# Kernel tuning notes

Hardware: AMD Instinct MI355X
Metric: run time of the kernel (lower is better)

## Reference

```python
import jax, jax.numpy as jnp
import numpy as np

DIM = 2048
K_DIM = 2048
HQ = 16          # query heads
HKV = 4          # kv heads
HD = DIM // HQ   # head dim = 128
KV_DIM = HD * HKV
MAX_LEN = 4096
THETA = 10000.0
ROPE_FACTOR = 8.0
CAUSAL = True
SCALE = HD ** -0.5


def rope_cos_sin(n):
    # mirrors generate_sin_cos_pos_emb (rope_factor > 1 branch)
    idx = jnp.arange(0, HD, 2, dtype=jnp.float32) / HD
    seq_len_eff = max(n, MAX_LEN)  # static python ints
    base_adjustment = (ROPE_FACTOR * seq_len_eff / MAX_LEN - (ROPE_FACTOR - 1.0)) ** (HD / (HD - 2))
    inv_freq = 1.0 / (THETA * base_adjustment) ** idx
    pos = jnp.arange(n, dtype=jnp.float32)
    if not CAUSAL:
        pos = pos - (n - 1) // 2
    freqs = pos[:, None] * inv_freq[None, :]          # [n, HD/2]
    emb = jnp.concatenate([freqs, freqs], axis=-1)    # [n, HD]
    return jnp.cos(emb), jnp.sin(emb)


def rotate_half(x):
    x1, x2 = jnp.split(x, 2, axis=-1)
    return jnp.concatenate([-x2, x1], axis=-1)


def setup_inputs() -> dict:
    key = jax.random.key(0)
    ks = jax.random.split(key, 11)
    B, N = 2, 2048
    s = 0.02
    return {
        "query": jax.random.normal(ks[0], (B, N, DIM), jnp.float32),
        "key": jax.random.normal(ks[1], (B, N, K_DIM), jnp.float32),
        "value": jax.random.normal(ks[2], (B, N, K_DIM), jnp.float32),
        "Wq": jax.random.normal(ks[3], (DIM, DIM), jnp.float32) * s,
        "bq": jnp.zeros((DIM,), jnp.float32),
        "Wk": jax.random.normal(ks[4], (KV_DIM, K_DIM), jnp.float32) * s,
        "bk": jnp.zeros((KV_DIM,), jnp.float32),
        "Wv": jax.random.normal(ks[5], (KV_DIM, K_DIM), jnp.float32) * s,
        "bv": jnp.zeros((KV_DIM,), jnp.float32),
        "Wo": jax.random.normal(ks[6], (DIM, DIM), jnp.float32) * s,
        "bo": jnp.zeros((DIM,), jnp.float32),
    }


def reference(query, key, value, Wq, bq, Wk, bk, Wv, bv, Wo, bo):
    b, n, _ = query.shape
    q = query @ Wq.T + bq                       # [b, n, DIM]
    k = key @ Wk.T + bk                         # [b, n, KV_DIM]
    v = value @ Wv.T + bv                       # [b, n, KV_DIM]
    q = q.reshape(b, n, HQ, HD).transpose(0, 2, 1, 3)    # [b, HQ, n, d]
    k = k.reshape(b, n, HKV, HD).transpose(0, 2, 1, 3)   # [b, HKV, n, d]
    v = v.reshape(b, n, HKV, HD).transpose(0, 2, 1, 3)
    cos, sin = rope_cos_sin(n)                  # [n, HD] each, broadcast over b,h
    q = q * cos + rotate_half(q) * sin
    k = k * cos + rotate_half(k) * sin
    g = HQ // HKV
    qg = q.reshape(b, HKV, g, n, HD)            # group query heads per kv head
    scores = jnp.einsum('bhgnd,bhsd->bhgns', qg * SCALE, k)  # [b, HKV, g, n, s]
    if CAUSAL:
        causal = jnp.tril(jnp.ones((n, n), dtype=bool))
        scores = jnp.where(causal[None, None, None], scores, jnp.finfo(scores.dtype).min)
    attn = jax.nn.softmax(scores, axis=-1)
    out = jnp.einsum('bhgns,bhsd->bhgnd', attn, v)           # [b, HKV, g, n, d]
    out = out.reshape(b, HQ, n, HD).transpose(0, 2, 1, 3).reshape(b, n, DIM)
    return out @ Wo.T + bo
```

## Files before the change

### kernel.cpp

```cpp
#include <hip/hip_runtime.h>
#include <cstdint>


typedef __bf16 bf16_t;
typedef __attribute__((ext_vector_type(8))) __bf16 bf16x8;
typedef __attribute__((ext_vector_type(4))) float f32x4;

#define B_    2
#define N_    2048
#define DIM_  2048
#define HQ_   16
#define HKV_  4
#define HD_   128
#define KVD_  512
#define SCALE_ 0.08838834764831845f

static __device__ __forceinline__ void ld_g2l(void* lds, const void* g) {
  __builtin_amdgcn_global_load_lds((__attribute__((address_space(1))) void*)g,
                                   (__attribute__((address_space(3))) void*)lds,
                                   16, 0, 0);
}

static __device__ __forceinline__ f32x4 vmax4(f32x4 a, f32x4 b) {
  f32x4 r;
  r[0] = fmaxf(a[0], b[0]); r[1] = fmaxf(a[1], b[1]);
  r[2] = fmaxf(a[2], b[2]); r[3] = fmaxf(a[3], b[3]);
  return r;
}

__global__ void k_sincos(float* __restrict__ cosT, float* __restrict__ sinT) {
  int idx = blockIdx.x * 256 + threadIdx.x;
  int i = idx & 63;
  int n = idx >> 6;
  float inv = expf(-(float)i * (9.210340371976184f / 64.0f));
  float ang = (float)n * inv;
  cosT[idx] = cosf(ang);
  sinT[idx] = sinf(ang);
}

__global__ void k_cvt4(const float* __restrict__ s0, bf16_t* __restrict__ d0, int n0,
                       const float* __restrict__ s1, bf16_t* __restrict__ d1, int n1,
                       const float* __restrict__ s2, bf16_t* __restrict__ d2, int n2,
                       const float* __restrict__ s3, bf16_t* __restrict__ d3, int n3)
{
  int i = (blockIdx.x * 256 + threadIdx.x) * 4;
  const float* s; bf16_t* d; int off;
  if (i < n0)                     { s = s0; d = d0; off = i; }
  else if (i < n0 + n1)           { s = s1; d = d1; off = i - n0; }
  else if (i < n0 + n1 + n2)      { s = s2; d = d2; off = i - n0 - n1; }
  else if (i < n0 + n1 + n2 + n3) { s = s3; d = d3; off = i - n0 - n1 - n2; }
  else return;
  f32x4 v = *(const f32x4*)(s + off);
  union { bf16_t h[4]; uint2 u; } pk;
  pk.h[0] = (bf16_t)v[0]; pk.h[1] = (bf16_t)v[1];
  pk.h[2] = (bf16_t)v[2]; pk.h[3] = (bf16_t)v[3];
  *(uint2*)(d + off) = pk.u;
}

__global__ __launch_bounds__(256, 2) void k_gemm_qkv(
    const float* __restrict__ q, const bf16_t* __restrict__ Wqb,
    const float* __restrict__ bq, bf16_t* __restrict__ Qp,
    const float* __restrict__ k, const bf16_t* __restrict__ Wkb,
    const float* __restrict__ bk, bf16_t* __restrict__ Kp,
    const float* __restrict__ v, const bf16_t* __restrict__ Wvb,
    const float* __restrict__ bv, bf16_t* __restrict__ Vp)
{
  __shared__ bf16_t As[128 * 64];
  __shared__ bf16_t Bs[2][128 * 64];
  const int z = blockIdx.z;
  if (z != 0 && blockIdx.y >= 2) return;
  const float* A; const bf16_t* W; const float* bias; bf16_t* C; int Nn;
  if (z == 0)      { A = q; W = Wqb; bias = bq; C = Qp; Nn = 2048; }
  else if (z == 1) { A = k; W = Wkb; bias = bk; C = Kp; Nn = 512; }
  else             { A = v; W = Wvb; bias = bv; C = Vp; Nn = 512; }

  const int tid  = threadIdx.x;
  const int lane = tid & 63;
  const int wave = tid >> 6;
  const int l15  = lane & 15;
  const int lg   = lane >> 4;
  const int bm = blockIdx.x;
  const int bn0 = blockIdx.y * 2, bn1 = bn0 + 1;
  const int wr = (wave >> 1) * 64, wc = (wave & 1) * 64;
  const int K = 2048;

  f32x4 acc0[4][4] = {};
  f32x4 acc1[4][4] = {};

  uint8_t* AsB = (uint8_t*)As;
  uint8_t* Bs0 = (uint8_t*)Bs[0];
  uint8_t* Bs1 = (uint8_t*)Bs[1];
  const uint8_t* Wb0 = (const uint8_t*)W + (size_t)(bn0 * 128) * K * 2;
  const uint8_t* Wb1 = (const uint8_t*)W + (size_t)(bn1 * 128) * K * 2;

  f32x4 arLo[4], arHi[4];

  auto loadA = [&](int k0) {
#pragma unroll
    for (int i = 0; i < 4; ++i) {
      int c = i * 256 + tid;
      int row = c >> 3;
      int k8  = (c & 7) * 8;
      const float* ap = A + (size_t)(bm * 128 + row) * K + k0 + k8;
      arLo[i] = *(const f32x4*)ap;
      arHi[i] = *(const f32x4*)(ap + 4);
    }
  };
  auto writeA = [&]() {
#pragma unroll
    for (int i = 0; i < 4; ++i) {
      int c = i * 256 + tid;
      int row = c >> 3;
      int k8  = (c & 7) * 8;
      bf16x8 va;
      f32x4 lo = arLo[i], hi = arHi[i];
      va[0] = (bf16_t)lo[0]; va[1] = (bf16_t)lo[1];
      va[2] = (bf16_t)lo[2]; va[3] = (bf16_t)lo[3];
      va[4] = (bf16_t)hi[0]; va[5] = (bf16_t)hi[1];
      va[6] = (bf16_t)hi[2]; va[7] = (bf16_t)hi[3];
      int sw = (k8 * 2) ^ ((row & 7) << 4);
      *(bf16x8*)(AsB + row * 128 + sw) = va;
    }
  };

  loadA(0);

  for (int k0 = 0; k0 < K; k0 += 64) {
#pragma unroll
    for (int r = 0; r < 4; ++r) {
      int o = r * 4096 + wave * 1024 + lane * 16;
      int row = o >> 7;
      int colB = (o & 127) ^ ((row & 7) << 4);
      size_t goff = (size_t)row * (K * 2) + (size_t)k0 * 2 + colB;
      ld_g2l(Bs0 + r * 4096 + wave * 1024, Wb0 + goff);
      ld_g2l(Bs1 + r * 4096 + wave * 1024, Wb1 + goff);
    }
    writeA();
    __syncthreads();
    if (k0 + 64 < K) loadA(k0 + 64);
    __builtin_amdgcn_s_setprio(1);
#pragma unroll
    for (int kk = 0; kk < 2; ++kk) {
      const int koff = kk * 64 + (lg << 4);
      bf16x8 fa[4], fb[4];
#pragma unroll
      for (int fi = 0; fi < 4; ++fi) {
        int row = wr + fi * 16 + l15;
        fa[fi] = *(const bf16x8*)(AsB + row * 128 + (koff ^ ((row & 7) << 4)));
      }
#pragma unroll
      for (int fj = 0; fj < 4; ++fj) {
        int row = wc + fj * 16 + l15;
        fb[fj] = *(const bf16x8*)(Bs0 + row * 128 + (koff ^ ((row & 7) << 4)));
      }
#pragma unroll
      for (int fi = 0; fi < 4; ++fi)
#pragma unroll
        for (int fj = 0; fj < 4; ++fj)
          acc0[fi][fj] = __builtin_amdgcn_mfma_f32_16x16x32_bf16(
              fa[fi], fb[fj], acc0[fi][fj], 0, 0, 0);
#pragma unroll
      for (int fj = 0; fj < 4; ++fj) {
        int row = wc + fj * 16 + l15;
        fb[fj] = *(const bf16x8*)(Bs1 + row * 128 + (koff ^ ((row & 7) << 4)));
      }
#pragma unroll
      for (int fi = 0; fi < 4; ++fi)
#pragma unroll
        for (int fj = 0; fj < 4; ++fj)
          acc1[fi][fj] = __builtin_amdgcn_mfma_f32_16x16x32_bf16(
              fa[fi], fb[fj], acc1[fi][fj], 0, 0, 0);
    }
    __builtin_amdgcn_s_setprio(0);
    __syncthreads();
  }

  const int r0 = lg * 4;
#pragma unroll
  for (int fi = 0; fi < 4; ++fi) {
#pragma unroll
    for (int rr = 0; rr < 4; ++rr) {
      int grow = bm * 128 + wr + fi * 16 + r0 + rr;
      size_t rowoff = (size_t)grow * Nn;
#pragma unroll
      for (int fj = 0; fj < 4; ++fj) {
        int gc0 = bn0 * 128 + wc + fj * 16 + l15;
        int gc1 = bn1 * 128 + wc + fj * 16 + l15;
        C[rowoff + gc0] = (bf16_t)(acc0[fi][fj][rr] + bias[gc0]);
        C[rowoff + gc1] = (bf16_t)(acc1[fi][fj][rr] + bias[gc1]);
      }
    }
  }
}

__global__ __launch_bounds__(256, 4) void k_gemm_o(
    const bf16_t* __restrict__ Ain, const bf16_t* __restrict__ Wob,
    const float* __restrict__ bo, float* __restrict__ out)
{
  __shared__ bf16_t As[128 * 64];
  __shared__ bf16_t Bs[128 * 64];
  const int tid  = threadIdx.x;
  const int lane = tid & 63;
  const int wave = tid >> 6;
  const int l15  = lane & 15;
  const int lg   = lane >> 4;
  const int bm = blockIdx.x, bn = blockIdx.y;
  const int wr = (wave >> 1) * 64, wc = (wave & 1) * 64;
  const int K = 2048, N = 2048;

  f32x4 acc[4][4] = {};
  uint8_t* AsB = (uint8_t*)As;
  uint8_t* BsB = (uint8_t*)Bs;
  const uint8_t* Wbase = (const uint8_t*)Wob + (size_t)(bn * 128) * K * 2;
  const uint8_t* Abase = (const uint8_t*)Ain + (size_t)(bm * 128) * K * 2;

  for (int k0 = 0; k0 < K; k0 += 64) {
    for (int r = 0; r < 4; ++r) {
      int o = r * 4096 + wave * 1024 + lane * 16;
      int row = o >> 7;
      int colB = (o & 127) ^ ((row & 7) << 4);
      size_t goff = (size_t)row * (K * 2) + (size_t)k0 * 2 + colB;
      ld_g2l(BsB + r * 4096 + wave * 1024, Wbase + goff);
      ld_g2l(AsB + r * 4096 + wave * 1024, Abase + goff);
    }
    __syncthreads();
    for (int kk = 0; kk < 2; ++kk) {
      const int koff = kk * 64 + (lg << 4);
      bf16x8 fa[4], fb[4];
      for (int fi = 0; fi < 4; ++fi) {
        int row = wr + fi * 16 + l15;
        fa[fi] = *(const bf16x8*)(AsB + row * 128 + (koff ^ ((row & 7) << 4)));
      }
      for (int fj = 0; fj < 4; ++fj) {
        int row = wc + fj * 16 + l15;
        fb[fj] = *(const bf16x8*)(BsB + row * 128 + (koff ^ ((row & 7) << 4)));
      }
      for (int fi = 0; fi < 4; ++fi)
        for (int fj = 0; fj < 4; ++fj)
          acc[fi][fj] = __builtin_amdgcn_mfma_f32_16x16x32_bf16(
              fa[fi], fb[fj], acc[fi][fj], 0, 0, 0);
    }
    __syncthreads();
  }

  const int r0 = lg * 4;
  for (int fi = 0; fi < 4; ++fi) {
    for (int rr = 0; rr < 4; ++rr) {
      int grow = bm * 128 + wr + fi * 16 + r0 + rr;
      size_t rowoff = (size_t)grow * N;
      for (int fj = 0; fj < 4; ++fj) {
        int gcol = bn * 128 + wc + fj * 16 + l15;
        out[rowoff + gcol] = acc[fi][fj][rr] + bo[gcol];
      }
    }
  }
}

__global__ void k_ropek_transv(bf16_t* __restrict__ Kp,
                               const float* __restrict__ cosT,
                               const float* __restrict__ sinT,
                               const bf16_t* __restrict__ Vp,
                               bf16_t* __restrict__ Vt)
{
  __shared__ bf16_t tile[64][72];
  const int tid = threadIdx.x;
  if (blockIdx.x < 512) {
    int idx = blockIdx.x * 256 + tid;
    int j = idx & 7;
    int h = (idx >> 3) & 3;
    int row = idx >> 5;
    int n = row & (N_ - 1);
    int d0 = j * 8;
    const float* cp = cosT + (n << 6) + d0;
    const float* sp = sinT + (n << 6) + d0;
    f32x4 c0 = *(const f32x4*)cp,  c1 = *(const f32x4*)(cp + 4);
    f32x4 s0 = *(const f32x4*)sp,  s1 = *(const f32x4*)(sp + 4);
    bf16_t* xb = Kp + (size_t)row * 512 + (h << 7) + d0;
    bf16x8 x1 = *(const bf16x8*)xb;
    bf16x8 x2 = *(const bf16x8*)(xb + 64);
    bf16x8 o1, o2;
#pragma unroll
    for (int e = 0; e < 8; ++e) {
      float c = e < 4 ? c0[e] : c1[e - 4];
      float s = e < 4 ? s0[e] : s1[e - 4];
      float a = (float)x1[e], bvl = (float)x2[e];
      o1[e] = (bf16_t)(a * c - bvl * s);
      o2[e] = (bf16_t)(bvl * c + a * s);
    }
    *(bf16x8*)xb = o1;
    *(bf16x8*)(xb + 64) = o2;
    return;
  }
  const int bid = blockIdx.x - 512;
  const int r0 = (bid & 63) * 64;
  const int d0 = (bid >> 6) * 64;
  for (int r = 0; r < 2; ++r) {
    int n = r * 32 + (tid >> 3);
    int dc = (tid & 7) * 8;
    *(uint4*)&tile[n][dc] = *(const uint4*)(Vp + (size_t)(r0 + n) * KVD_ + d0 + dc);
  }
  __syncthreads();
  const int b = r0 >> 11;
  const int nseq = r0 & (N_ - 1);
  for (int r = 0; r < 2; ++r) {
    int dd = r * 32 + (tid >> 3);
    int nc = (tid & 7) * 8;
    int dglob = d0 + dd;
    int hkv = dglob >> 7, dloc = dglob & 127;
    union { bf16_t h[8]; uint4 v; } pk;
    for (int j = 0; j < 8; ++j) pk.h[j] = tile[nc + j][dd];
    size_t drow = (size_t)(b * HKV_ + hkv) * 128 + dloc;
    *(uint4*)(Vt + drow * N_ + nseq + nc) = pk.v;
  }
}

__global__ __launch_bounds__(256, 2) void k_attn(
    const bf16_t* __restrict__ Qp, const bf16_t* __restrict__ Kp,
    const bf16_t* __restrict__ Vt, bf16_t* __restrict__ AO,
    const float* __restrict__ cosT, const float* __restrict__ sinT)
{
  __shared__ bf16_t Ks[2][64 * 128];
  __shared__ bf16_t Vs[2][128 * 64];
  __shared__ bf16_t Ps[4][16 * 72];
  const int tid = threadIdx.x, lane = tid & 63, wave = tid >> 6;
  const int l15 = lane & 15, lg = lane >> 4;
  const int bx = (blockIdx.y < 16) ? (15 - (int)blockIdx.x) : (int)blockIdx.x;
  const int qtile = bx * 4 + wave;
  const int bh = blockIdx.y;
  const int b = bh >> 4, hq = bh & 15, hkv = hq >> 2;

  bf16x8 qf[2][4];
#pragma unroll
  for (int rf = 0; rf < 2; ++rf) {
    int n = qtile * 32 + rf * 16 + l15;
    size_t qrow = (size_t)b * N_ + n;
    const uint8_t* qb = (const uint8_t*)Qp + (qrow * DIM_ + (size_t)hq * HD_) * 2 + lg * 16;
#pragma unroll
    for (int ks = 0; ks < 4; ++ks)
      qf[rf][ks] = *(const bf16x8*)(qb + ks * 64);
    const float* cb = cosT + n * 64 + lg * 8;
    const float* sb = sinT + n * 64 + lg * 8;
    f32x4 c0a = *(const f32x4*)cb,        c0b = *(const f32x4*)(cb + 4);
    f32x4 c1a = *(const f32x4*)(cb + 32), c1b = *(const f32x4*)(cb + 36);
    f32x4 s0a = *(const f32x4*)sb,        s0b = *(const f32x4*)(sb + 4);
    f32x4 s1a = *(const f32x4*)(sb + 32), s1b = *(const f32x4*)(sb + 36);
#pragma unroll
    for (int e = 0; e < 8; ++e) {
      float c0 = e < 4 ? c0a[e] : c0b[e - 4], s0 = e < 4 ? s0a[e] : s0b[e - 4];
      float c1 = e < 4 ? c1a[e] : c1b[e - 4], s1 = e < 4 ? s1a[e] : s1b[e - 4];
      float a0 = (float)qf[rf][0][e], b0 = (float)qf[rf][2][e];
      float a1 = (float)qf[rf][1][e], b1 = (float)qf[rf][3][e];
      qf[rf][0][e] = (bf16_t)((a0 * c0 - b0 * s0) * SCALE_);
      qf[rf][2][e] = (bf16_t)((b0 * c0 + a0 * s0) * SCALE_);
      qf[rf][1][e] = (bf16_t)((a1 * c1 - b1 * s1) * SCALE_);
      qf[rf][3][e] = (bf16_t)((b1 * c1 + a1 * s1) * SCALE_);
    }
  }

  float m[2] = {-1e30f, -1e30f};
  float ln[2] = {0.f, 0.f};
  f32x4 o[2][8] = {};

  const uint8_t* KpB = (const uint8_t*)Kp + ((size_t)b * N_ * KVD_ + (size_t)hkv * HD_) * 2;
  const uint8_t* VtB = (const uint8_t*)Vt + (size_t)(b * HKV_ + hkv) * HD_ * (size_t)N_ * 2;
  uint8_t* PwB = (uint8_t*)Ps[wave];

  const int Tw   = qtile / 2 + 1;
  const int Tmax = 2 * bx + 2;

  auto stage = [&](int buf, int t) {
    uint8_t* KsB = (uint8_t*)Ks[buf];
    uint8_t* VsB = (uint8_t*)Vs[buf];
#pragma unroll
    for (int r = 0; r < 4; ++r) {
      int o16 = r * 4096 + wave * 1024 + lane * 16;
      int row = o16 >> 8;
      int colB = (o16 & 255) ^ ((row & 7) << 4);
      ld_g2l(KsB + r * 4096 + wave * 1024,
             KpB + (size_t)(t * 64 + row) * (KVD_ * 2) + colB);
    }
#pragma unroll
    for (int r = 0; r < 4; ++r) {
      int o16 = r * 4096 + wave * 1024 + lane * 16;
      int dd = o16 >> 7;
      int colB = (o16 & 127) ^ ((dd & 7) << 4);
      ld_g2l(VsB + r * 4096 + wave * 1024,
             VtB + (size_t)dd * (N_ * 2) + t * 128 + colB);
    }
  };

  stage(0, 0);
  __syncthreads();
  int cur = 0;

  for (int t = 0; t < Tmax; ++t) {
    if (t + 1 < Tmax) stage(cur ^ 1, t + 1);

    if (t < Tw) {
      const uint8_t* KsB = (const uint8_t*)Ks[cur];
      const uint8_t* VsB = (const uint8_t*)Vs[cur];

      f32x4 s4[2][4] = {};
      __builtin_amdgcn_s_setprio(1);
#pragma unroll
      for (int ks = 0; ks < 4; ++ks) {
        int koff = ks * 64 + lg * 16;
#pragma unroll
        for (int kb = 0; kb < 4; ++kb) {
          int row = kb * 16 + l15;
          bf16x8 kf = *(const bf16x8*)(KsB + row * 256 + (koff ^ ((row & 7) << 4)));
          s4[0][kb] = __builtin_amdgcn_mfma_f32_16x16x32_bf16(kf, qf[0][ks], s4[0][kb], 0, 0, 0);
          s4[1][kb] = __builtin_amdgcn_mfma_f32_16x16x32_bf16(kf, qf[1][ks], s4[1][kb], 0, 0, 0);
        }
      }
      __builtin_amdgcn_s_setprio(0);

      if (t == Tw - 1) {
#pragma unroll
        for (int rf = 0; rf < 2; ++rf) {
          int q = qtile * 32 + rf * 16 + l15;
#pragma unroll
          for (int kb = 0; kb < 4; ++kb) {
            int key = t * 64 + kb * 16 + lg * 4;
#pragma unroll
            for (int rr = 0; rr < 4; ++rr)
              if (key + rr > q) s4[rf][kb][rr] = -1e30f;
          }
        }
      }

      bf16x8 pf[2][2];
#pragma unroll
      for (int rf = 0; rf < 2; ++rf) {
        f32x4 mx = vmax4(vmax4(s4[rf][0], s4[rf][1]), vmax4(s4[rf][2], s4[rf][3]));
        float rm = fmaxf(fmaxf(mx[0], mx[1]), fmaxf(mx[2], mx[3]));
        rm = fmaxf(rm, __shfl_xor(rm, 16));
        rm = fmaxf(rm, __shfl_xor(rm, 32));

        const bool defer = __all(rm <= m[rf] + 8.0f);
        float mn = defer ? m[rf] : fmaxf(m[rf], rm);
        float sc = defer ? 1.0f : __expf(m[rf] - mn);

        f32x4 p[4];
        f32x4 psum = {0.f, 0.f, 0.f, 0.f};
#pragma unroll
        for (int kb = 0; kb < 4; ++kb) {
#pragma unroll
          for (int rr = 0; rr < 4; ++rr)
            p[kb][rr] = __expf(s4[rf][kb][rr] - mn);
          psum += p[kb];
        }
        float rs = (psum[0] + psum[1]) + (psum[2] + psum[3]);
        rs += __shfl_xor(rs, 16);
        rs += __shfl_xor(rs, 32);
        ln[rf] = ln[rf] * sc + rs;
        m[rf] = mn;

        if (!defer) {
#pragma unroll
          for (int db = 0; db < 8; ++db) o[rf][db] *= sc;
        }

#pragma unroll
        for (int kb = 0; kb < 4; ++kb) {
          union { bf16_t h[4]; uint2 u; } pk;
          pk.h[0] = (bf16_t)p[kb][0]; pk.h[1] = (bf16_t)p[kb][1];
          pk.h[2] = (bf16_t)p[kb][2]; pk.h[3] = (bf16_t)p[kb][3];
          *(uint2*)(PwB + l15 * 144 + kb * 32 + lg * 8) = pk.u;
        }
        pf[rf][0] = *(const bf16x8*)(PwB + l15 * 144 + lg * 16);
        pf[rf][1] = *(const bf16x8*)(PwB + l15 * 144 + 64 + lg * 16);
      }

      __builtin_amdgcn_s_setprio(1);
#pragma unroll
      for (int ks2 = 0; ks2 < 2; ++ks2) {
        int koff = ks2 * 64 + lg * 16;
#pragma unroll
        for (int db = 0; db < 8; ++db) {
          int dd = db * 16 + l15;
          bf16x8 vf = *(const bf16x8*)(VsB + dd * 128 + (koff ^ ((dd & 7) << 4)));
          o[0][db] = __builtin_amdgcn_mfma_f32_16x16x32_bf16(vf, pf[0][ks2], o[0][db], 0, 0, 0);
          o[1][db] = __builtin_amdgcn_mfma_f32_16x16x32_bf16(vf, pf[1][ks2], o[1][db], 0, 0, 0);
        }
      }
      __builtin_amdgcn_s_setprio(0);
    }

    __syncthreads();
    cur ^= 1;
  }

#pragma unroll
  for (int rf = 0; rf < 2; ++rf) {
    float iv = 1.f / ln[rf];
    size_t qrow = (size_t)b * N_ + qtile * 32 + rf * 16 + l15;
    uint8_t* ob = (uint8_t*)(AO + qrow * DIM_ + (size_t)hq * HD_);
#pragma unroll
    for (int db = 0; db < 8; ++db) {
      union { bf16_t h[4]; uint2 u; } pk;
      pk.h[0] = (bf16_t)(o[rf][db][0] * iv);
      pk.h[1] = (bf16_t)(o[rf][db][1] * iv);
      pk.h[2] = (bf16_t)(o[rf][db][2] * iv);
      pk.h[3] = (bf16_t)(o[rf][db][3] * iv);
      *(uint2*)(ob + (db * 16 + lg * 4) * 2) = pk.u;
    }
  }
}

extern "C" void kernel_launch(void* const* d_in, const int* in_sizes, int n_in,
                              void* d_out, int out_size, void* d_ws, size_t ws_size,
                              hipStream_t stream)
{
  if (ws_size < (46u << 20)) return;

  const float* query = (const float*)d_in[0];
  const float* key   = (const float*)d_in[1];
  const float* value = (const float*)d_in[2];
  const float* Wq = (const float*)d_in[3];
  const float* bq = (const float*)d_in[4];
  const float* Wk = (const float*)d_in[5];
  const float* bk = (const float*)d_in[6];
  const float* Wv = (const float*)d_in[7];
  const float* bv = (const float*)d_in[8];
  const float* Wo = (const float*)d_in[9];
  const float* bo = (const float*)d_in[10];
  float* out = (float*)d_out;

  uint8_t* ws = (uint8_t*)d_ws;
  float*  cosT = (float*)(ws);
  float*  sinT = (float*)(ws + (512u << 10));
  bf16_t* Qp   = (bf16_t*)(ws + (1u  << 20));
  bf16_t* Kp   = (bf16_t*)(ws + (17u << 20));
  bf16_t* Vp   = (bf16_t*)(ws + (21u << 20));
  bf16_t* Vt   = (bf16_t*)(ws + (25u << 20));
  bf16_t* Wqb  = (bf16_t*)(ws + (29u << 20));
  bf16_t* Wkb  = (bf16_t*)(ws + (37u << 20));
  bf16_t* Wvb  = (bf16_t*)(ws + (39u << 20));
  bf16_t* WobL = (bf16_t*)(ws + (17u << 20));
  bf16_t* WobE = (bf16_t*)(ws + (41u << 20));

  const bool bigws = ws_size >= (50ull << 20);

  k_sincos<<<512, 256, 0, stream>>>(cosT, sinT);

  if (bigws) {
    k_cvt4<<<10240, 256, 0, stream>>>(Wq, Wqb, 4194304,
                                      Wk, Wkb, 1048576,
                                      Wv, Wvb, 1048576,
                                      Wo, WobE, 4194304);
  } else {
    k_cvt4<<<6144, 256, 0, stream>>>(Wq, Wqb, 4194304,
                                     Wk, Wkb, 1048576,
                                     Wv, Wvb, 1048576,
                                     nullptr, nullptr, 0);
  }

  k_gemm_qkv<<<dim3(32, 8, 3), 256, 0, stream>>>(
      query, Wqb, bq, Qp, key, Wkb, bk, Kp, value, Wvb, bv, Vp);

  k_ropek_transv<<<1024, 256, 0, stream>>>(Kp, cosT, sinT, Vp, Vt);

  k_attn<<<dim3(16, 32), 256, 0, stream>>>(Qp, Kp, Vt, Qp, cosT, sinT);

  if (!bigws) {
    k_cvt4<<<4096, 256, 0, stream>>>(Wo, WobL, 4194304,
                                     nullptr, nullptr, 0,
                                     nullptr, nullptr, 0,
                                     nullptr, nullptr, 0);
  }

  k_gemm_o<<<dim3(32, 16), 256, 0, stream>>>(
      Qp, bigws ? WobE : WobL, bo, out);
}
```

Before: 204.0 us.

## Double-buffer weight and activation LDS tiles in QKV and output GEMMs

Both projection GEMMs now keep two LDS buffers and issue the async global-to-LDS loads for the next K-slice before running MFMAs on the current one, so memory latency can overlap with compute. The output GEMM also gains unroll pragmas and setprio hints, and its occupancy target drops from 4 to 2 blocks per CU. The cost is doubled LDS per block (QKV goes to about 80KB), which may cut occupancy. Correctness also depends on the global_load_lds writes being complete by the single barrier per iteration, since no explicit vmcnt wait is added.

```diff
diff --git a/kernel.cpp b/kernel.cpp
--- a/kernel.cpp
+++ b/kernel.cpp
@@ -66,7 +66,7 @@
     const float* __restrict__ bv, bf16_t* __restrict__ Vp)
 {
   __shared__ bf16_t As[128 * 64];
-  __shared__ bf16_t Bs[2][128 * 64];
+  __shared__ bf16_t Bs[2][2][128 * 64];
   const int z = blockIdx.z;
   if (z != 0 && blockIdx.y >= 2) return;
   const float* A; const bf16_t* W; const float* bias; bf16_t* C; int Nn;
@@ -88,8 +88,6 @@
   f32x4 acc1[4][4] = {};
 
   uint8_t* AsB = (uint8_t*)As;
-  uint8_t* Bs0 = (uint8_t*)Bs[0];
-  uint8_t* Bs1 = (uint8_t*)Bs[1];
   const uint8_t* Wb0 = (const uint8_t*)W + (size_t)(bn0 * 128) * K * 2;
   const uint8_t* Wb1 = (const uint8_t*)W + (size_t)(bn1 * 128) * K * 2;
 
@@ -122,22 +120,33 @@
       *(bf16x8*)(AsB + row * 128 + sw) = va;
     }
   };
-
-  loadA(0);
-
-  for (int k0 = 0; k0 < K; k0 += 64) {
+  auto stageW = [&](int buf, int k0) {
+    uint8_t* B0 = (uint8_t*)Bs[buf][0];
+    uint8_t* B1 = (uint8_t*)Bs[buf][1];
 #pragma unroll
     for (int r = 0; r < 4; ++r) {
       int o = r * 4096 + wave * 1024 + lane * 16;
       int row = o >> 7;
       int colB = (o & 127) ^ ((row & 7) << 4);
       size_t goff = (size_t)row * (K * 2) + (size_t)k0 * 2 + colB;
-      ld_g2l(Bs0 + r * 4096 + wave * 1024, Wb0 + goff);
-      ld_g2l(Bs1 + r * 4096 + wave * 1024, Wb1 + goff);
-    }
+      ld_g2l(B0 + r * 4096 + wave * 1024, Wb0 + goff);
+      ld_g2l(B1 + r * 4096 + wave * 1024, Wb1 + goff);
+    }
+  };
+
+  loadA(0);
+  stageW(0, 0);
+  int cur = 0;
+
+  for (int k0 = 0; k0 < K; k0 += 64) {
     writeA();
     __syncthreads();
-    if (k0 + 64 < K) loadA(k0 + 64);
+    if (k0 + 64 < K) {
+      loadA(k0 + 64);
+      stageW(cur ^ 1, k0 + 64);
+    }
+    const uint8_t* B0 = (const uint8_t*)Bs[cur][0];
+    const uint8_t* B1 = (const uint8_t*)Bs[cur][1];
     __builtin_amdgcn_s_setprio(1);
 #pragma unroll
     for (int kk = 0; kk < 2; ++kk) {
@@ -151,7 +160,7 @@
 #pragma unroll
       for (int fj = 0; fj < 4; ++fj) {
         int row = wc + fj * 16 + l15;
-        fb[fj] = *(const bf16x8*)(Bs0 + row * 128 + (koff ^ ((row & 7) << 4)));
+        fb[fj] = *(const bf16x8*)(B0 + row * 128 + (koff ^ ((row & 7) << 4)));
       }
 #pragma unroll
       for (int fi = 0; fi < 4; ++fi)
@@ -162,7 +171,7 @@
 #pragma unroll
       for (int fj = 0; fj < 4; ++fj) {
         int row = wc + fj * 16 + l15;
-        fb[fj] = *(const bf16x8*)(Bs1 + row * 128 + (koff ^ ((row & 7) << 4)));
+        fb[fj] = *(const bf16x8*)(B1 + row * 128 + (koff ^ ((row & 7) << 4)));
       }
 #pragma unroll
       for (int fi = 0; fi < 4; ++fi)
@@ -173,6 +182,7 @@
     }
     __builtin_amdgcn_s_setprio(0);
     __syncthreads();
+    cur ^= 1;
   }
 
   const int r0 = lg * 4;
@@ -193,12 +203,12 @@
   }
 }
 
-__global__ __launch_bounds__(256, 4) void k_gemm_o(
+__global__ __launch_bounds__(256, 2) void k_gemm_o(
     const bf16_t* __restrict__ Ain, const bf16_t* __restrict__ Wob,
     const float* __restrict__ bo, float* __restrict__ out)
 {
-  __shared__ bf16_t As[128 * 64];
-  __shared__ bf16_t Bs[128 * 64];
+  __shared__ bf16_t As[2][128 * 64];
+  __shared__ bf16_t Bs[2][128 * 64];
   const int tid  = threadIdx.x;
   const int lane = tid & 63;
   const int wave = tid >> 6;
@@ -209,45 +219,66 @@
   const int K = 2048, N = 2048;
 
   f32x4 acc[4][4] = {};
-  uint8_t* AsB = (uint8_t*)As;
-  uint8_t* BsB = (uint8_t*)Bs;
   const uint8_t* Wbase = (const uint8_t*)Wob + (size_t)(bn * 128) * K * 2;
   const uint8_t* Abase = (const uint8_t*)Ain + (size_t)(bm * 128) * K * 2;
 
-  for (int k0 = 0; k0 < K; k0 += 64) {
+  auto stage = [&](int buf, int k0) {
+    uint8_t* Ad = (uint8_t*)As[buf];
+    uint8_t* Bd = (uint8_t*)Bs[buf];
+#pragma unroll
     for (int r = 0; r < 4; ++r) {
       int o = r * 4096 + wave * 1024 + lane * 16;
       int row = o >> 7;
       int colB = (o & 127) ^ ((row & 7) << 4);
       size_t goff = (size_t)row * (K * 2) + (size_t)k0 * 2 + colB;
-      ld_g2l(BsB + r * 4096 + wave * 1024, Wbase + goff);
-      ld_g2l(AsB + r * 4096 + wave * 1024, Abase + goff);
-    }
-    __syncthreads();
+      ld_g2l(Bd + r * 4096 + wave * 1024, Wbase + goff);
+      ld_g2l(Ad + r * 4096 + wave * 1024, Abase + goff);
+    }
+  };
+
+  stage(0, 0);
+  __syncthreads();
+  int cur = 0;
+
+  for (int k0 = 0; k0 < K; k0 += 64) {
+    if (k0 + 64 < K) stage(cur ^ 1, k0 + 64);
+    const uint8_t* Ar = (const uint8_t*)As[cur];
+    const uint8_t* Br = (const uint8_t*)Bs[cur];
+    __builtin_amdgcn_s_setprio(1);
+#pragma unroll
     for (int kk = 0; kk < 2; ++kk) {
       const int koff = kk * 64 + (lg << 4);
       bf16x8 fa[4], fb[4];
+#pragma unroll
       for (int fi = 0; fi < 4; ++fi) {
         int row = wr + fi * 16 + l15;
-        fa[fi] = *(const bf16x8*)(AsB + row * 128 + (koff ^ ((row & 7) << 4)));
-      }
+        fa[fi] = *(const bf16x8*)(Ar + row * 128 + (koff ^ ((row & 7) << 4)));
+      }
+#pragma unroll
       for (int fj = 0; fj < 4; ++fj) {
         int row = wc + fj * 16 + l15;
-        fb[fj] = *(const bf16x8*)(BsB + row * 128 + (koff ^ ((row & 7) << 4)));
-      }
+        fb[fj] = *(const bf16x8*)(Br + row * 128 + (koff ^ ((row & 7) << 4)));
+      }
+#pragma unroll
       for (int fi = 0; fi < 4; ++fi)
+#pragma unroll
         for (int fj = 0; fj < 4; ++fj)
           acc[fi][fj] = __builtin_amdgcn_mfma_f32_16x16x32_bf16(
               fa[fi], fb[fj], acc[fi][fj], 0, 0, 0);
     }
+    __builtin_amdgcn_s_setprio(0);
     __syncthreads();
+    cur ^= 1;
   }
 
   const int r0 = lg * 4;
+#pragma unroll
   for (int fi = 0; fi < 4; ++fi) {
+#pragma unroll
     for (int rr = 0; rr < 4; ++rr) {
       int grow = bm * 128 + wr + fi * 16 + r0 + rr;
       size_t rowoff = (size_t)grow * N;
+#pragma unroll
       for (int fj = 0; fj < 4; ++fj) {
         int gcol = bn * 128 + wc + fj * 16 + l15;
         out[rowoff + gcol] = acc[fi][fj][rr] + bo[gcol];
```

Measured after the change: 206.3 us. About the same (+1.1%).
